# Kernel optimization log

Hardware: AMD Instinct MI355X
Metric: run time of the kernel (lower is better)

The kernel has to match this reference:

```python
import jax, jax.numpy as jnp
from jax import lax
import numpy as np

B, DM, NL, NC = 4, 256, 4, 1000
DI, NS, DTR, K = 512, 16, 32, 4  # d_inner, d_state, dt_rank, d_conv
EPS = 1e-5


def _bn(x, g, b):
    # eval-mode BatchNorm2d with running stats (mean=0, var=1)
    return x * (g / jnp.sqrt(1.0 + EPS))[None, :, None, None] + b[None, :, None, None]


def _conv2d(x, w, b, stride, pad):
    y = lax.conv_general_dilated(x, w, (stride, stride), pad,
                                 dimension_numbers=('NCHW', 'OIHW', 'NCHW'))
    return y + b[None, :, None, None]


def _ln(x, g, b):
    m = x.mean(-1, keepdims=True)
    v = ((x - m) ** 2).mean(-1, keepdims=True)
    return (x - m) / jnp.sqrt(v + EPS) * g + b


def _selective_scan(u, delta, A, Bm, Cm, D):
    # u, delta: [b,d,l]; A: [d,n]; Bm, Cm: [b,n,l]; D: [d]
    dA = jnp.exp(jnp.einsum('bdl,dn->lbdn', delta, A))        # [l,b,d,n]
    dBu = jnp.einsum('bdl,bnl,bdl->lbdn', delta, Bm, u)       # [l,b,d,n]
    h0 = jnp.zeros(dA.shape[1:], u.dtype)

    def step(h, inp):
        a, bu = inp
        h = a * h + bu
        return h, h

    _, hs = lax.scan(step, h0, (dA, dBu))                     # [l,b,d,n]
    y = jnp.einsum('lbdn,bnl->bdl', hs, Cm)
    return y + u * D[None, :, None]


def _mamba_block(x, ipw, ipb, cw, cb, xpw, dpw, dpb, alog, dssm, opw, opb):
    # x: [b,l,d_model]
    xr = x @ ipw.T + ipb                                      # [b,l,2*DI]
    xi, res = jnp.split(xr, 2, axis=-1)
    xc = jnp.swapaxes(xi, 1, 2)                               # [b,DI,l]
    # depthwise conv1d, kernel 4, torch padding='same' -> pad (1,2)
    xc = lax.conv_general_dilated(xc, cw, (1,), [(1, 2)],
                                  dimension_numbers=('NCW', 'OIW', 'NCW'),
                                  feature_group_count=DI) + cb[None, :, None]
    xl = jnp.swapaxes(xc, 1, 2)                               # [b,l,DI]
    xdbl = xl @ xpw.T                                         # [b,l,DTR+2*NS]
    d_dt, Bs, Cs = jnp.split(xdbl, [DTR, DTR + NS], axis=-1)
    delta = jax.nn.softplus(d_dt @ dpw.T + dpb)               # [b,l,DI]
    A = -jnp.exp(alog)                                        # [DI,NS]
    y = _selective_scan(jnp.swapaxes(xl, 1, 2), jnp.swapaxes(delta, 1, 2), A,
                        jnp.swapaxes(Bs, 1, 2), jnp.swapaxes(Cs, 1, 2), dssm)
    y = jnp.swapaxes(y, 1, 2)                                 # [b,l,DI]
    y = y * jax.nn.silu(res)
    return y @ opw.T + opb


def setup_inputs() -> dict:
    key = jax.random.key(0)
    ks = iter(jax.random.split(key, 32))

    def rn(shape, scale=0.02):
        return jax.random.normal(next(ks), shape, jnp.float32) * scale

    inp = {
        'x': jax.random.normal(next(ks), (B, 3, 64, 64), jnp.float32),
        # conv stem
        'c1w': rn((DM // 2, 3, 3, 3)), 'c1b': jnp.zeros((DM // 2,)),
        'g1': jnp.ones((DM // 2,)), 'b1': jnp.zeros((DM // 2,)),
        'c2w': rn((DM, DM // 2, 3, 3)), 'c2b': jnp.zeros((DM,)),
        'g2': jnp.ones((DM,)), 'b2': jnp.zeros((DM,)),
        'pw': rn((DM, DM, 2, 2)), 'pb': jnp.zeros((DM,)),
        'g3': jnp.ones((DM,)), 'b3': jnp.zeros((DM,)),
        # stacked mamba block params [NL, ...]
        'ipw': rn((NL, 2 * DI, DM)), 'ipb': jnp.zeros((NL, 2 * DI)),
        'cw': rn((NL, DI, 1, K), 0.1), 'cb': jnp.zeros((NL, DI)),
        'xpw': rn((NL, DTR + 2 * NS, DI)),
        'dpw': rn((NL, DI, DTR)), 'dpb': rn((NL, DI), 0.1),
        'alog': jnp.broadcast_to(jnp.log(jnp.arange(1, NS + 1, dtype=jnp.float32)), (NL, DI, NS)),
        'dssm': jnp.ones((NL, DI)),
        'opw': rn((NL, DM, DI)), 'opb': jnp.zeros((NL, DM)),
        'lnw': jnp.ones((NL, DM)), 'lnb': jnp.zeros((NL, DM)),
        # head
        'nw': jnp.ones((DM,)), 'nb': jnp.zeros((DM,)),
        'fcw': rn((NC, DM)), 'fcb': jnp.zeros((NC,)),
    }
    return inp


def reference(x, c1w, c1b, g1, b1, c2w, c2b, g2, b2, pw, pb, g3, b3,
              ipw, ipb, cw, cb, xpw, dpw, dpb, alog, dssm, opw, opb,
              lnw, lnb, nw, nb, fcw, fcb):
    h = _conv2d(x, c1w, c1b, 1, [(1, 1), (1, 1)])
    h = jax.nn.gelu(_bn(h, g1, b1), approximate=False)
    h = _conv2d(h, c2w, c2b, 1, [(1, 1), (1, 1)])
    h = jax.nn.gelu(_bn(h, g2, b2), approximate=False)
    h = _conv2d(h, pw, pb, 2, [(0, 0), (0, 0)])
    h = jax.nn.gelu(_bn(h, g3, b3), approximate=False)
    b, c, H, W = h.shape
    s = h.reshape(b, c, H * W).transpose(0, 2, 1)             # [b, L, d_model]
    for i in range(NL):
        y = _mamba_block(s, ipw[i], ipb[i], cw[i], cb[i], xpw[i], dpw[i],
                         dpb[i], alog[i], dssm[i], opw[i], opb[i])
        s = _ln(y, lnw[i], lnb[i]) + s
    s = s.mean(axis=1)
    s = _ln(s, nw, nb)
    logits = s @ fcw.T + fcb
    return logits, jax.nn.softmax(logits, axis=-1)
```

## Files before the change

### kernel.cpp

```cpp
#include <hip/hip_runtime.h>
#include <math.h>


#define BN_RSQ 0.99999500003749969f

typedef unsigned int uint;
typedef unsigned short ushort;
typedef __bf16 bf16x8 __attribute__((ext_vector_type(8)));
typedef float floatx4 __attribute__((ext_vector_type(4)));

__device__ __forceinline__ float gelu_f(float v) {
    return 0.5f * v * (1.0f + erff(v * 0.70710678118654752f));
}
__device__ __forceinline__ float softplus_f(float v) {
    return (v > 20.f) ? v : log1pf(expf(v));
}
__device__ __forceinline__ ushort f2bf(float f) {
    uint x = __float_as_uint(f);
    x += 0x7fffu + ((x >> 16) & 1u);
    return (ushort)(x >> 16);
}
__device__ __forceinline__ float bf2f(ushort u) {
    return __uint_as_float((uint)u << 16);
}

#define DPP_ROW_SHR_ADD(x, N)                                               \
    x += __int_as_float(__builtin_amdgcn_update_dpp(                        \
        0, __float_as_int(x), 0x110 + (N), 0xf, 0xf, true))

__global__ void wprep(const float* __restrict__ ipw, const float* __restrict__ opw,
                      const float* __restrict__ c2w, const float* __restrict__ pw,
                      const float* __restrict__ xpw,
                      ushort* __restrict__ ipwb, ushort* __restrict__ opwb,
                      ushort* __restrict__ w2b, ushort* __restrict__ pwTb,
                      ushort* __restrict__ xpwb)
{
    int idx = blockIdx.x * 256 + threadIdx.x;
    if (idx < 1048576) {
        ipwb[idx] = f2bf(ipw[idx]);
    } else if (idx < 1572864) {
        int i = idx - 1048576;
        opwb[i] = f2bf(opw[i]);
    } else if (idx < 1867776) {
        int i = idx - 1572864;
        int oc = i / 1152, k = i % 1152;
        int s = k >> 7, ic = k & 127;
        w2b[i] = f2bf(c2w[(size_t)(oc * 128 + ic) * 9 + s]);
    } else if (idx < 2129920) {
        int i = idx - 1867776;
        int oc = i >> 10, k = i & 1023;
        int s = k >> 8, ic = k & 255;
        int ky = s >> 1, kx = s & 1;
        pwTb[i] = f2bf(pw[((size_t)(oc * 256 + ic) * 2 + ky) * 2 + kx]);
    } else if (idx < 2260992) {
        int i = idx - 2129920;
        xpwb[i] = f2bf(xpw[i]);
    }
}

__global__ __launch_bounds__(256) void conv1_nhwc(
    const float* __restrict__ x, const float* __restrict__ w,
    const float* __restrict__ cb, const float* __restrict__ g,
    const float* __restrict__ bb, ushort* __restrict__ out)
{
    __shared__ float tin[3][3][64];
    __shared__ float ws[3456];
    int t = threadIdx.x;
    int b = blockIdx.x >> 6, y = blockIdx.x & 63;
    for (int i = t; i < 3456; i += 256) ws[i] = w[i];
    for (int i = t; i < 576; i += 256) {
        int ic = i / 192, r = (i >> 6) % 3, xx = i & 63;
        int gy = y + r - 1;
        tin[ic][r][xx] = ((unsigned)gy < 64u) ? x[((b * 3 + ic) * 64 + gy) * 64 + xx] : 0.f;
    }
    __syncthreads();
    int tx = t & 15, ty = t >> 4;
    int oc0 = tx * 8, px0 = ty * 4;
    float acc[4][8];
    #pragma unroll
    for (int p = 0; p < 4; ++p)
        #pragma unroll
        for (int o = 0; o < 8; ++o) acc[p][o] = 0.f;
    for (int ic = 0; ic < 3; ++ic)
        #pragma unroll
        for (int ky = 0; ky < 3; ++ky)
            #pragma unroll
            for (int kx = 0; kx < 3; ++kx) {
                float av[4];
                #pragma unroll
                for (int p = 0; p < 4; ++p) {
                    int xx = px0 + p + kx - 1;
                    av[p] = ((unsigned)xx < 64u) ? tin[ic][ky][xx] : 0.f;
                }
                #pragma unroll
                for (int o = 0; o < 8; ++o) {
                    float wv = ws[(oc0 + o) * 27 + ic * 9 + ky * 3 + kx];
                    #pragma unroll
                    for (int p = 0; p < 4; ++p) acc[p][o] = fmaf(av[p], wv, acc[p][o]);
                }
            }
    #pragma unroll
    for (int p = 0; p < 4; ++p) {
        uint pk[4];
        #pragma unroll
        for (int o2 = 0; o2 < 4; ++o2) {
            int oc = oc0 + o2 * 2;
            float v0 = gelu_f((acc[p][o2 * 2] + cb[oc]) * (g[oc] * BN_RSQ) + bb[oc]);
            float v1 = gelu_f((acc[p][o2 * 2 + 1] + cb[oc + 1]) * (g[oc + 1] * BN_RSQ) + bb[oc + 1]);
            pk[o2] = (uint)f2bf(v0) | ((uint)f2bf(v1) << 16);
        }
        uint4 vv = make_uint4(pk[0], pk[1], pk[2], pk[3]);
        *(uint4*)(out + ((size_t)((b * 64 + y) * 64 + px0 + p)) * 128 + oc0) = vv;
    }
}

template<int BM, int BN, int EPI>
__global__ __launch_bounds__(256, 2) void mfma_gemm_bt(
    const ushort* __restrict__ A, int lda,
    const ushort* __restrict__ W, int ldw,
    const float* __restrict__ bias,
    const float* __restrict__ bnG, const float* __restrict__ bnB,
    float* __restrict__ Cf, ushort* __restrict__ Cb, ushort* __restrict__ Cb2,
    int ldc, int K)
{
    constexpr int PAD = 40;
    constexpr int AP = BM / 64;
    constexpr int BP = BN / 64;
    constexpr int FM = BM / 32;
    constexpr int FN = BN / 32;
    __shared__ __align__(16) ushort As[BM * PAD];
    __shared__ __align__(16) ushort Bs[BN * PAD];
    int t = threadIdx.x;
    int m0 = blockIdx.x * BM, n0 = blockIdx.y * BN;
    int lane = t & 63, wid = t >> 6;
    int wm = (wid & 1) * (BM / 2), wn = (wid >> 1) * (BN / 2);
    int fr = lane & 15, fk = (lane >> 4) * 8;
    int r0 = t >> 2, c0 = (t & 3) * 8;
    floatx4 acc[FM][FN];
    #pragma unroll
    for (int i = 0; i < FM; ++i)
        #pragma unroll
        for (int j = 0; j < FN; ++j) acc[i][j] = {0.f, 0.f, 0.f, 0.f};
    uint4 ra[AP], rb[BP];
    #pragma unroll
    for (int p = 0; p < AP; ++p)
        ra[p] = *(const uint4*)(A + (size_t)(m0 + r0 + p * 64) * lda + c0);
    #pragma unroll
    for (int p = 0; p < BP; ++p)
        rb[p] = *(const uint4*)(W + (size_t)(n0 + r0 + p * 64) * ldw + c0);
    for (int k0 = 0; k0 < K; k0 += 32) {
        __syncthreads();
        #pragma unroll
        for (int p = 0; p < AP; ++p) *(uint4*)&As[(r0 + p * 64) * PAD + c0] = ra[p];
        #pragma unroll
        for (int p = 0; p < BP; ++p) *(uint4*)&Bs[(r0 + p * 64) * PAD + c0] = rb[p];
        __syncthreads();
        if (k0 + 32 < K) {
            #pragma unroll
            for (int p = 0; p < AP; ++p)
                ra[p] = *(const uint4*)(A + (size_t)(m0 + r0 + p * 64) * lda + k0 + 32 + c0);
            #pragma unroll
            for (int p = 0; p < BP; ++p)
                rb[p] = *(const uint4*)(W + (size_t)(n0 + r0 + p * 64) * ldw + k0 + 32 + c0);
        }
        bf16x8 af[FM], bw[FN];
        #pragma unroll
        for (int i = 0; i < FM; ++i)
            af[i] = *(const bf16x8*)&As[(wm + i * 16 + fr) * PAD + fk];
        #pragma unroll
        for (int j = 0; j < FN; ++j)
            bw[j] = *(const bf16x8*)&Bs[(wn + j * 16 + fr) * PAD + fk];
        #pragma unroll
        for (int i = 0; i < FM; ++i)
            #pragma unroll
            for (int j = 0; j < FN; ++j)
                acc[i][j] = __builtin_amdgcn_mfma_f32_16x16x32_bf16(af[i], bw[j], acc[i][j], 0, 0, 0);
    }
    int rbase = (lane >> 4) * 4, cc = lane & 15;
    #pragma unroll
    for (int j = 0; j < FN; ++j) {
        int n = n0 + wn + j * 16 + cc;
        float bv = bias ? bias[n] : 0.f;
        float scl = 0.f, shf = 0.f;
        if (EPI == 2) { scl = bnG[n] * BN_RSQ; shf = bnB[n]; }
        #pragma unroll
        for (int i = 0; i < FM; ++i) {
            #pragma unroll
            for (int r = 0; r < 4; ++r) {
                int m = m0 + wm + i * 16 + rbase + r;
                float v = acc[i][j][r] + bv;
                if (EPI == 2) v = gelu_f(v * scl + shf);
                if (EPI == 0) {
                    Cf[(size_t)m * ldc + n] = v;
                } else if (EPI == 2) {
                    Cf[(size_t)m * ldc + n] = v;
                    Cb[(size_t)m * ldc + n] = f2bf(v);
                } else {
                    if (n < 512) Cb[(size_t)m * 512 + n] = f2bf(v);
                    else Cb2[(size_t)m * 512 + (n - 512)] = f2bf(v / (1.f + __expf(-v)));
                }
            }
        }
    }
}

#define C2_LOAD(step)                                                            \
    {                                                                            \
        int s_ = (step) >> 1, ich_ = ((step) & 1) * 64;                          \
        int ky_ = s_ / 3, kx_ = s_ % 3;                                          \
        int sy_ = y0 + (ra_row >> 6) + ky_ - 1;                                  \
        int sx_ = (ra_row & 63) + kx_ - 1;                                       \
        bool v_ = ((unsigned)sy_ < 64u) && ((unsigned)sx_ < 64u);                \
        const ushort* ap_ = hb + ((size_t)(sy_ * 64 + sx_)) * 128 + ich_ + ra_c; \
        uint4 zz_ = make_uint4(0u, 0u, 0u, 0u);                                  \
        ra0 = v_ ? *(const uint4*)(ap_ + 0)  : zz_;                              \
        ra1 = v_ ? *(const uint4*)(ap_ + 8)  : zz_;                              \
        ra2 = v_ ? *(const uint4*)(ap_ + 16) : zz_;                              \
        ra3 = v_ ? *(const uint4*)(ap_ + 24) : zz_;                              \
        const ushort* wp_ = w2b + (size_t)(n0 + rb_row) * 1152 + s_ * 128 + ich_ + rb_c; \
        rb0 = *(const uint4*)(wp_ + 0);                                          \
        rb1 = *(const uint4*)(wp_ + 8);                                          \
    }

__global__ __launch_bounds__(256, 2) void conv2_mfma(
    const ushort* __restrict__ h1b, const ushort* __restrict__ w2b,
    const float* __restrict__ cb, const float* __restrict__ g,
    const float* __restrict__ bb, ushort* __restrict__ h2b)
{
    constexpr int PAD = 72;
    __shared__ __align__(16) ushort As[128 * PAD];
    __shared__ __align__(16) ushort Bs[64 * PAD];
    int t = threadIdx.x;
    int m0 = blockIdx.x * 128, n0 = blockIdx.y * 64;
    int b = m0 >> 12;
    int y0 = (m0 & 4095) >> 6;
    int lane = t & 63, wid = t >> 6;
    int wm = (wid & 1) * 64, wn = (wid >> 1) * 32;
    int fr = lane & 15, fk = (lane >> 4) * 8;
    int ra_row = t >> 1, ra_c = (t & 1) * 32;
    int rb_row = t >> 2, rb_c = (t & 3) * 16;
    floatx4 acc[4][2];
    #pragma unroll
    for (int i = 0; i < 4; ++i)
        #pragma unroll
        for (int j = 0; j < 2; ++j) acc[i][j] = {0.f, 0.f, 0.f, 0.f};
    const ushort* hb = h1b + (size_t)b * 4096 * 128;

    uint4 ra0, ra1, ra2, ra3, rb0, rb1;
    C2_LOAD(0);
    for (int step = 0; step < 18; ++step) {
        __syncthreads();
        *(uint4*)&As[ra_row * PAD + ra_c + 0]  = ra0;
        *(uint4*)&As[ra_row * PAD + ra_c + 8]  = ra1;
        *(uint4*)&As[ra_row * PAD + ra_c + 16] = ra2;
        *(uint4*)&As[ra_row * PAD + ra_c + 24] = ra3;
        *(uint4*)&Bs[rb_row * PAD + rb_c + 0]  = rb0;
        *(uint4*)&Bs[rb_row * PAD + rb_c + 8]  = rb1;
        __syncthreads();
        if (step + 1 < 18) C2_LOAD(step + 1);
        #pragma unroll
        for (int ks = 0; ks < 64; ks += 32) {
            bf16x8 af[4], bw[2];
            #pragma unroll
            for (int i = 0; i < 4; ++i)
                af[i] = *(const bf16x8*)&As[(wm + i * 16 + fr) * PAD + ks + fk];
            #pragma unroll
            for (int j = 0; j < 2; ++j)
                bw[j] = *(const bf16x8*)&Bs[(wn + j * 16 + fr) * PAD + ks + fk];
            #pragma unroll
            for (int i = 0; i < 4; ++i)
                #pragma unroll
                for (int j = 0; j < 2; ++j)
                    acc[i][j] = __builtin_amdgcn_mfma_f32_16x16x32_bf16(af[i], bw[j], acc[i][j], 0, 0, 0);
        }
    }
    int rbase = (lane >> 4) * 4, cc = lane & 15;
    #pragma unroll
    for (int j = 0; j < 2; ++j) {
        int n = n0 + wn + j * 16 + cc;
        float scl = g[n] * BN_RSQ, shf = bb[n], bv2 = cb[n];
        #pragma unroll
        for (int i = 0; i < 4; ++i) {
            #pragma unroll
            for (int r = 0; r < 4; ++r) {
                int m = m0 + wm + i * 16 + rbase + r;
                float v = gelu_f((acc[i][j][r] + bv2) * scl + shf);
                h2b[(size_t)m * 256 + n] = f2bf(v);
            }
        }
    }
}

__global__ void im2col_bf16(const ushort* __restrict__ h2b, ushort* __restrict__ Apb)
{
    int idx = blockIdx.x * 256 + threadIdx.x;
    int k8 = idx & 127;
    int m = idx >> 7;
    int b = m >> 10, oy = (m >> 5) & 31, ox = m & 31;
    int s = k8 >> 5, ic8 = k8 & 31;
    int ky = s >> 1, kx = s & 1;
    uint4 v = *(const uint4*)(h2b + ((size_t)(b * 4096 + (2 * oy + ky) * 64 + 2 * ox + kx)) * 256 + ic8 * 8);
    *(uint4*)(Apb + (size_t)m * 1024 + k8 * 8) = v;
}

template<int BM, int BN, int BK, int TM, int TN>
__global__ __launch_bounds__(256) void gemm_kernel(
    const float* __restrict__ A, int lda,
    const float* __restrict__ W, int ldw,
    const float* __restrict__ bias,
    float* __restrict__ C, int ldc,
    int M, int N, int K, int act)
{
    static_assert(BM * BK / 4 == 256 && BN * BK / 4 == 256, "staging shape");
    __shared__ float As[BK][BM + 4];
    __shared__ float Bs[BK][BN + 4];
    int t = threadIdx.x;
    int m0 = blockIdx.x * BM, n0 = blockIdx.y * BN;
    float acc[TM][TN];
    #pragma unroll
    for (int i = 0; i < TM; i++)
        #pragma unroll
        for (int j = 0; j < TN; j++) acc[i][j] = 0.f;
    const int LPR = BK / 4;
    int lr = t / LPR, lc4 = (t % LPR) * 4;
    int ty = t >> 4, tx = t & 15;
    int ma = m0 + lr, nb = n0 + lr;
    float4 va = make_float4(0.f, 0.f, 0.f, 0.f);
    float4 vb = make_float4(0.f, 0.f, 0.f, 0.f);
    if (ma < M) va = *(const float4*)(A + (size_t)ma * lda + lc4);
    if (nb < N) vb = *(const float4*)(W + (size_t)nb * ldw + lc4);
    for (int k0 = 0; k0 < K; k0 += BK) {
        __syncthreads();
        As[lc4 + 0][lr] = va.x; As[lc4 + 1][lr] = va.y;
        As[lc4 + 2][lr] = va.z; As[lc4 + 3][lr] = va.w;
        Bs[lc4 + 0][lr] = vb.x; Bs[lc4 + 1][lr] = vb.y;
        Bs[lc4 + 2][lr] = vb.z; Bs[lc4 + 3][lr] = vb.w;
        __syncthreads();
        if (k0 + BK < K) {
            if (ma < M) va = *(const float4*)(A + (size_t)ma * lda + k0 + BK + lc4);
            if (nb < N) vb = *(const float4*)(W + (size_t)nb * ldw + k0 + BK + lc4);
        }
        #pragma unroll
        for (int kk = 0; kk < BK; ++kk) {
            float a[TM], bfr[TN];
            #pragma unroll
            for (int i = 0; i < TM; i += 4)
                *(float4*)&a[i] = *(const float4*)&As[kk][ty * TM + i];
            #pragma unroll
            for (int j = 0; j < TN; j += 4)
                *(float4*)&bfr[j] = *(const float4*)&Bs[kk][tx * TN + j];
            #pragma unroll
            for (int i = 0; i < TM; i++)
                #pragma unroll
                for (int j = 0; j < TN; j++) acc[i][j] = fmaf(a[i], bfr[j], acc[i][j]);
        }
    }
    #pragma unroll
    for (int i = 0; i < TM; i++) {
        int m = m0 + ty * TM + i;
        if (m >= M) continue;
        #pragma unroll
        for (int j = 0; j < TN; j++) {
            int n = n0 + tx * TN + j;
            if (n >= N) continue;
            float v = acc[i][j];
            if (bias) v += bias[n];
            if (act == 2) v = softplus_f(v);
            C[(size_t)m * ldc + n] = v;
        }
    }
}

__global__ __launch_bounds__(256) void dwconv(
    const ushort* __restrict__ xib, const float* __restrict__ cw,
    const float* __restrict__ cb, ushort* __restrict__ xlb)
{
    int idx = blockIdx.x * 256 + threadIdx.x;
    int d4 = (idx & 127) * 4;
    int bl = idx >> 7;
    int b = bl >> 10, l = bl & 1023;
    float4 w0 = *(const float4*)(cw + d4 * 4);
    float4 w1 = *(const float4*)(cw + d4 * 4 + 4);
    float4 w2 = *(const float4*)(cw + d4 * 4 + 8);
    float4 w3 = *(const float4*)(cw + d4 * 4 + 12);
    float4 acc = *(const float4*)(cb + d4);
    const ushort* rowb = xib + ((size_t)b << 19) + d4;
    #pragma unroll
    for (int k = 0; k < 4; ++k) {
        int ll = l + k - 1;
        if ((unsigned)ll < 1024u) {
            uint2 p = *(const uint2*)(rowb + (size_t)ll * 512);
            acc.x = fmaf(bf2f((ushort)(p.x & 0xffffu)), ((const float*)&w0)[k], acc.x);
            acc.y = fmaf(bf2f((ushort)(p.x >> 16)),     ((const float*)&w1)[k], acc.y);
            acc.z = fmaf(bf2f((ushort)(p.y & 0xffffu)), ((const float*)&w2)[k], acc.z);
            acc.w = fmaf(bf2f((ushort)(p.y >> 16)),     ((const float*)&w3)[k], acc.w);
        }
    }
    uint2 pk;
    pk.x = (uint)f2bf(acc.x) | ((uint)f2bf(acc.y) << 16);
    pk.y = (uint)f2bf(acc.z) | ((uint)f2bf(acc.w) << 16);
    *(uint2*)(xlb + (size_t)bl * 512 + d4) = pk;
}

__global__ __launch_bounds__(512, 8) void scan_part1(
    const float* __restrict__ xdbl, const ushort* __restrict__ xlb,
    const float* __restrict__ dpw, const float* __restrict__ dpb,
    const float* __restrict__ alog,
    float* __restrict__ Psum, float* __restrict__ hFsum)
{
    __shared__ __align__(16) float Td[32][68];
    __shared__ __align__(16) float Tu[32][68];
    __shared__ __align__(16) float TB[16][68];
    __shared__ __align__(16) float xd[64][32];
    __shared__ float dpw_s[32][33];
    __shared__ float dpb_s[32];
    int t = threadIdx.x;
    int bid = blockIdx.x;
    int ch = bid % 15;
    int gq = bid / 15;
    int dgG = gq & 15, b = gq >> 4;
    int d0 = dgG * 32;
    int bl0 = b * 1024 + ch * 64;
    {
        int l = t >> 3, k4 = (t & 7) * 4;
        float4 v = *(const float4*)(xdbl + (size_t)(bl0 + l) * 64 + k4);
        *(float4*)&xd[l][k4] = v;
    }
    if (t < 256) {
        int l = t >> 2, d8 = (t & 3) * 8;
        uint4 p = *(const uint4*)(xlb + (size_t)(bl0 + l) * 512 + d0 + d8);
        Tu[d8 + 0][l] = bf2f((ushort)(p.x & 0xffffu));
        Tu[d8 + 1][l] = bf2f((ushort)(p.x >> 16));
        Tu[d8 + 2][l] = bf2f((ushort)(p.y & 0xffffu));
        Tu[d8 + 3][l] = bf2f((ushort)(p.y >> 16));
        Tu[d8 + 4][l] = bf2f((ushort)(p.z & 0xffffu));
        Tu[d8 + 5][l] = bf2f((ushort)(p.z >> 16));
        Tu[d8 + 6][l] = bf2f((ushort)(p.w & 0xffffu));
        Tu[d8 + 7][l] = bf2f((ushort)(p.w >> 16));
    } else {
        int tt = t - 256;
        int l = tt >> 2, n4 = (tt & 3) * 4;
        float4 bv = *(const float4*)(xdbl + (size_t)(bl0 + l) * 64 + 32 + n4);
        TB[n4 + 0][l] = bv.x; TB[n4 + 1][l] = bv.y;
        TB[n4 + 2][l] = bv.z; TB[n4 + 3][l] = bv.w;
    }
    #pragma unroll
    for (int r = 0; r < 2; ++r) {
        int idx = r * 512 + t;
        int dd = idx >> 5, kk = idx & 31;
        dpw_s[dd][kk] = dpw[(size_t)(d0 + dd) * 32 + kk];
    }
    if (t < 32) dpb_s[t] = dpb[d0 + t];
    __syncthreads();
    {
        int dd = t & 31, lb = (t >> 5) * 4;
        #pragma unroll
        for (int j = 0; j < 4; ++j) {
            int l = lb + j;
            float s = dpb_s[dd];
            #pragma unroll
            for (int k = 0; k < 32; ++k) s = fmaf(xd[l][k], dpw_s[dd][k], s);
            Td[dd][l] = softplus_f(s);
        }
    }
    __syncthreads();
    int w = t >> 6, lane = t & 63;
    int dl = lane >> 4, n = lane & 15;
    int col = w * 4 + dl;
    int d = d0 + col;
    float Ac = -__expf(alog[d * 16 + n]);
    float h = 0.f, P = 1.f;
    for (int l4 = 0; l4 < 16; ++l4) {
        float4 de = *(const float4*)&Td[col][l4 * 4];
        float4 uu = *(const float4*)&Tu[col][l4 * 4];
        float4 Bv = *(const float4*)&TB[n][l4 * 4];
        float a1 = __expf(de.x * Ac), a2 = __expf(de.y * Ac);
        float a3 = __expf(de.z * Ac), a4 = __expf(de.w * Ac);
        float b1 = de.x * Bv.x * uu.x, b2 = de.y * Bv.y * uu.y;
        float b3 = de.z * Bv.z * uu.z, b4 = de.w * Bv.w * uu.w;
        float a21 = a2 * a1,     b21 = fmaf(a2, b1, b2);
        float a321 = a3 * a21,   b321 = fmaf(a3, b21, b3);
        float a4321 = a4 * a321, b4321 = fmaf(a4, b321, b4);
        h = fmaf(a4321, h, b4321);
        P *= a4321;
    }
    size_t si = ((size_t)(b * 128 + dgG * 8 + w) * 16 + ch) * 64 + lane;
    Psum[si] = P;
    hFsum[si] = h;
}

__global__ __launch_bounds__(512, 8) void scan_part2(
    const float* __restrict__ xdbl, const ushort* __restrict__ xlb,
    const float* __restrict__ dpw, const float* __restrict__ dpb,
    const float* __restrict__ alog, const float* __restrict__ dssm,
    const ushort* __restrict__ resb, ushort* __restrict__ ybb,
    const float* __restrict__ Psum, const float* __restrict__ hFsum)
{
    __shared__ __align__(16) float Td[32][68];
    __shared__ __align__(16) float Tu[32][68];
    __shared__ __align__(16) unsigned char uni[12928];
    __shared__ float dpw_s[32][33];
    __shared__ float dpb_s[32];
    float* xd = (float*)uni;
    float (*TB)[68] = (float(*)[68])uni;
    float (*TC)[68] = (float(*)[68])(uni + 4352);
    uint (*yb2)[33] = (uint(*)[33])(uni + 8704);
    int t = threadIdx.x;
    int bid = blockIdx.x;
    int ch = bid & 15, dgG = (bid >> 4) & 15, b = bid >> 8;
    int d0 = dgG * 32;
    int bl0 = b * 1024 + ch * 64;
    {
        int l = t >> 3, k4 = (t & 7) * 4;
        float4 v = *(const float4*)(xdbl + (size_t)(bl0 + l) * 64 + k4);
        *(float4*)&xd[l * 32 + k4] = v;
    }
    if (t < 256) {
        int l = t >> 2, d8 = (t & 3) * 8;
        uint4 p = *(const uint4*)(xlb + (size_t)(bl0 + l) * 512 + d0 + d8);
        Tu[d8 + 0][l] = bf2f((ushort)(p.x & 0xffffu));
        Tu[d8 + 1][l] = bf2f((ushort)(p.x >> 16));
        Tu[d8 + 2][l] = bf2f((ushort)(p.y & 0xffffu));
        Tu[d8 + 3][l] = bf2f((ushort)(p.y >> 16));
        Tu[d8 + 4][l] = bf2f((ushort)(p.z & 0xffffu));
        Tu[d8 + 5][l] = bf2f((ushort)(p.z >> 16));
        Tu[d8 + 6][l] = bf2f((ushort)(p.w & 0xffffu));
        Tu[d8 + 7][l] = bf2f((ushort)(p.w >> 16));
    }
    #pragma unroll
    for (int r = 0; r < 2; ++r) {
        int idx = r * 512 + t;
        int dd = idx >> 5, kk = idx & 31;
        dpw_s[dd][kk] = dpw[(size_t)(d0 + dd) * 32 + kk];
    }
    if (t < 32) dpb_s[t] = dpb[d0 + t];
    __syncthreads();
    {
        int dd = t & 31, lb = (t >> 5) * 4;
        #pragma unroll
        for (int j = 0; j < 4; ++j) {
            int l = lb + j;
            float s = dpb_s[dd];
            #pragma unroll
            for (int k = 0; k < 32; ++k) s = fmaf(xd[l * 32 + k], dpw_s[dd][k], s);
            Td[dd][l] = softplus_f(s);
        }
    }
    __syncthreads();
    if (t < 256) {
        int l = t >> 2, n4 = (t & 3) * 4;
        float4 bv = *(const float4*)(xdbl + (size_t)(bl0 + l) * 64 + 32 + n4);
        float4 cv = *(const float4*)(xdbl + (size_t)(bl0 + l) * 64 + 48 + n4);
        TB[n4 + 0][l] = bv.x; TB[n4 + 1][l] = bv.y;
        TB[n4 + 2][l] = bv.z; TB[n4 + 3][l] = bv.w;
        TC[n4 + 0][l] = cv.x; TC[n4 + 1][l] = cv.y;
        TC[n4 + 2][l] = cv.z; TC[n4 + 3][l] = cv.w;
    }
    int w = t >> 6, lane = t & 63;
    int dl = lane >> 4, n = lane & 15;
    int col = w * 4 + dl;
    int d = d0 + col;
    float Ac = -__expf(alog[d * 16 + n]);
    float Dd = dssm[d];
    float h = 0.f;
    {
        size_t sbase = (size_t)(b * 128 + dgG * 8 + w) * 1024 + lane;
        for (int cc = 0; cc < ch; ++cc) {
            float Pv = Psum[sbase + (size_t)cc * 64];
            float hv = hFsum[sbase + (size_t)cc * 64];
            h = Pv * h + hv;
        }
    }
    __syncthreads();
    for (int l4 = 0; l4 < 16; ++l4) {
        float4 de = *(const float4*)&Td[col][l4 * 4];
        float4 uu = *(const float4*)&Tu[col][l4 * 4];
        float4 Bv = *(const float4*)&TB[n][l4 * 4];
        float4 Cv = *(const float4*)&TC[n][l4 * 4];
        float a1 = __expf(de.x * Ac), a2 = __expf(de.y * Ac);
        float a3 = __expf(de.z * Ac), a4 = __expf(de.w * Ac);
        float b1 = de.x * Bv.x * uu.x, b2 = de.y * Bv.y * uu.y;
        float b3 = de.z * Bv.z * uu.z, b4 = de.w * Bv.w * uu.w;
        float a21 = a2 * a1,     b21 = fmaf(a2, b1, b2);
        float a321 = a3 * a21,   b321 = fmaf(a3, b21, b3);
        float a4321 = a4 * a321, b4321 = fmaf(a4, b321, b4);
        float h1 = fmaf(a1, h, b1);
        float h2 = fmaf(a21, h, b21);
        float h3 = fmaf(a321, h, b321);
        float h4 = fmaf(a4321, h, b4321);
        h = h4;
        float p0 = h1 * Cv.x, p1 = h2 * Cv.y, p2 = h3 * Cv.z, p3 = h4 * Cv.w;
        DPP_ROW_SHR_ADD(p0, 1); DPP_ROW_SHR_ADD(p0, 2);
        DPP_ROW_SHR_ADD(p0, 4); DPP_ROW_SHR_ADD(p0, 8);
        DPP_ROW_SHR_ADD(p1, 1); DPP_ROW_SHR_ADD(p1, 2);
        DPP_ROW_SHR_ADD(p1, 4); DPP_ROW_SHR_ADD(p1, 8);
        DPP_ROW_SHR_ADD(p2, 1); DPP_ROW_SHR_ADD(p2, 2);
        DPP_ROW_SHR_ADD(p2, 4); DPP_ROW_SHR_ADD(p2, 8);
        DPP_ROW_SHR_ADD(p3, 1); DPP_ROW_SHR_ADD(p3, 2);
        DPP_ROW_SHR_ADD(p3, 4); DPP_ROW_SHR_ADD(p3, 8);
        if (n == 15) {
            int l2 = l4 * 2;
            float y0 = fmaf(uu.x, Dd, p0), y1 = fmaf(uu.y, Dd, p1);
            float y2 = fmaf(uu.z, Dd, p2), y3 = fmaf(uu.w, Dd, p3);
            yb2[l2 + 0][col] = (uint)f2bf(y0) | ((uint)f2bf(y1) << 16);
            yb2[l2 + 1][col] = (uint)f2bf(y2) | ((uint)f2bf(y3) << 16);
        }
    }
    __syncthreads();
    size_t base = ((size_t)(b * 1024 + ch * 64)) * 512 + d0;
    #pragma unroll
    for (int j = 0; j < 2; ++j) {
        int idx = j * 512 + t;
        int l2 = idx >> 5, col2 = idx & 31;
        uint yv = yb2[l2][col2];
        int l0 = l2 * 2;
        float r0 = bf2f(resb[base + (size_t)l0 * 512 + col2]);
        float r1 = bf2f(resb[base + (size_t)(l0 + 1) * 512 + col2]);
        float y0 = bf2f((ushort)(yv & 0xffffu)) * r0;
        float y1 = bf2f((ushort)(yv >> 16)) * r1;
        ybb[base + (size_t)l0 * 512 + col2] = f2bf(y0);
        ybb[base + (size_t)(l0 + 1) * 512 + col2] = f2bf(y1);
    }
}

__global__ __launch_bounds__(256) void ln_res_kernel(
    const float* __restrict__ o, const float* __restrict__ g,
    const float* __restrict__ bb, float* __restrict__ s, ushort* __restrict__ sb)
{
    int row = blockIdx.x * 4 + (threadIdx.x >> 6);
    int lane = threadIdx.x & 63;
    const float4* orow = (const float4*)(o + (size_t)row * 256);
    float4 v = orow[lane];
    float sum = v.x + v.y + v.z + v.w;
    float sq = v.x * v.x + v.y * v.y + v.z * v.z + v.w * v.w;
    #pragma unroll
    for (int off = 1; off < 64; off <<= 1) {
        sum += __shfl_xor(sum, off);
        sq += __shfl_xor(sq, off);
    }
    float m = sum * (1.f / 256.f);
    float var = sq * (1.f / 256.f) - m * m;
    float rstd = rsqrtf(var + 1e-5f);
    float4 gg = ((const float4*)g)[lane];
    float4 bv = ((const float4*)bb)[lane];
    float4* srow = (float4*)(s + (size_t)row * 256);
    float4 sv = srow[lane];
    sv.x += (v.x - m) * rstd * gg.x + bv.x;
    sv.y += (v.y - m) * rstd * gg.y + bv.y;
    sv.z += (v.z - m) * rstd * gg.z + bv.z;
    sv.w += (v.w - m) * rstd * gg.w + bv.w;
    srow[lane] = sv;
    uint2 pk;
    pk.x = (uint)f2bf(sv.x) | ((uint)f2bf(sv.y) << 16);
    pk.y = (uint)f2bf(sv.z) | ((uint)f2bf(sv.w) << 16);
    *(uint2*)(sb + (size_t)row * 256 + lane * 4) = pk;
}

__global__ __launch_bounds__(256) void pool_ln_kernel(
    const float* __restrict__ s, const float* __restrict__ nw,
    const float* __restrict__ nb, float* __restrict__ sln)
{
    int b = blockIdx.x, c = threadIdx.x;
    const float* p = s + (size_t)b * 262144 + c;
    float acc = 0.f;
    for (int l = 0; l < 1024; ++l) acc += p[(size_t)l * 256];
    float pooled = acc * (1.f / 1024.f);
    __shared__ float rs[4], rq[4];
    float sum = pooled, sq = pooled * pooled;
    #pragma unroll
    for (int off = 1; off < 64; off <<= 1) {
        sum += __shfl_xor(sum, off);
        sq += __shfl_xor(sq, off);
    }
    int w = threadIdx.x >> 6;
    if ((threadIdx.x & 63) == 0) { rs[w] = sum; rq[w] = sq; }
    __syncthreads();
    sum = rs[0] + rs[1] + rs[2] + rs[3];
    sq = rq[0] + rq[1] + rq[2] + rq[3];
    float m = sum * (1.f / 256.f);
    float var = sq * (1.f / 256.f) - m * m;
    float rstd = rsqrtf(var + 1e-5f);
    sln[b * 256 + c] = (pooled - m) * rstd * nw[c] + nb[c];
}

__global__ __launch_bounds__(256) void softmax_kernel(float* __restrict__ out)
{
    int b = threadIdx.x >> 6, lane = threadIdx.x & 63;
    const float* lg = out + b * 1000;
    float v[16];
    float mx = -1e30f;
    #pragma unroll
    for (int j = 0; j < 16; ++j) {
        int i = lane + j * 64;
        v[j] = (i < 1000) ? lg[i] : -1e30f;
        mx = fmaxf(mx, v[j]);
    }
    #pragma unroll
    for (int off = 1; off < 64; off <<= 1) mx = fmaxf(mx, __shfl_xor(mx, off));
    float sum = 0.f;
    #pragma unroll
    for (int j = 0; j < 16; ++j) {
        int i = lane + j * 64;
        if (i < 1000) { v[j] = __expf(v[j] - mx); sum += v[j]; }
    }
    #pragma unroll
    for (int off = 1; off < 64; off <<= 1) sum += __shfl_xor(sum, off);
    float inv = 1.f / sum;
    float* so = out + 4000 + b * 1000;
    #pragma unroll
    for (int j = 0; j < 16; ++j) {
        int i = lane + j * 64;
        if (i < 1000) so[i] = v[j] * inv;
    }
}

extern "C" void kernel_launch(void* const* d_in, const int* in_sizes, int n_in,
                              void* d_out, int out_size, void* d_ws, size_t ws_size,
                              hipStream_t stream)
{
    const float* x    = (const float*)d_in[0];
    const float* c1w  = (const float*)d_in[1];
    const float* c1b  = (const float*)d_in[2];
    const float* g1   = (const float*)d_in[3];
    const float* b1   = (const float*)d_in[4];
    const float* c2w  = (const float*)d_in[5];
    const float* c2b  = (const float*)d_in[6];
    const float* g2   = (const float*)d_in[7];
    const float* b2   = (const float*)d_in[8];
    const float* pw   = (const float*)d_in[9];
    const float* pb   = (const float*)d_in[10];
    const float* g3   = (const float*)d_in[11];
    const float* b3   = (const float*)d_in[12];
    const float* ipw  = (const float*)d_in[13];
    const float* ipb  = (const float*)d_in[14];
    const float* cw   = (const float*)d_in[15];
    const float* cb   = (const float*)d_in[16];
    const float* xpw  = (const float*)d_in[17];
    const float* dpw  = (const float*)d_in[18];
    const float* dpb  = (const float*)d_in[19];
    const float* alog = (const float*)d_in[20];
    const float* dssm = (const float*)d_in[21];
    const float* opw  = (const float*)d_in[22];
    const float* opb  = (const float*)d_in[23];
    const float* lnw  = (const float*)d_in[24];
    const float* lnb  = (const float*)d_in[25];
    const float* nw   = (const float*)d_in[26];
    const float* nb   = (const float*)d_in[27];
    const float* fcw  = (const float*)d_in[28];
    const float* fcb  = (const float*)d_in[29];
    float* out = (float*)d_out;
    float* wsf = (float*)d_ws;

    float*  s_   = wsf;
    ushort* sb   = (ushort*)(wsf + 1048576);
    ushort* xib  = (ushort*)(wsf + 1572864);
    ushort* h2b  = (ushort*)(wsf + 1572864);
    float*  obuf = wsf + 1572864;
    ushort* resb = (ushort*)(wsf + 3670016);
    ushort* xlb  = (ushort*)(wsf + 4718592);
    ushort* ybb  = (ushort*)(wsf + 4718592);
    ushort* h1b  = (ushort*)(wsf + 4718592);
    ushort* Apb  = (ushort*)(wsf + 6815744);
    float*  xdbl = wsf + 8912896;
    ushort* ipwb = (ushort*)(wsf + 9175040);
    ushort* opwb = (ushort*)(wsf + 9699328);
    ushort* w2b  = (ushort*)(wsf + 9961472);
    ushort* pwTb = (ushort*)(wsf + 10108928);
    float*  sln  = wsf + 10240000;
    float*  Psum = wsf + 10241024;
    float*  hFsum= wsf + 10765312;
    ushort* xpwb = (ushort*)(wsf + 11289600);

    hipLaunchKernelGGL(wprep, dim3(8832), dim3(256), 0, stream,
                       ipw, opw, c2w, pw, xpw, ipwb, opwb, w2b, pwTb, xpwb);

    hipLaunchKernelGGL(conv1_nhwc, dim3(256), dim3(256), 0, stream, x, c1w, c1b, g1, b1, h1b);
    hipLaunchKernelGGL(conv2_mfma, dim3(128, 4), dim3(256), 0, stream, h1b, w2b, c2b, g2, b2, h2b);
    hipLaunchKernelGGL(im2col_bf16, dim3(2048), dim3(256), 0, stream, h2b, Apb);
    hipLaunchKernelGGL((mfma_gemm_bt<64, 64, 2>), dim3(64, 4), dim3(256), 0, stream,
                       Apb, 1024, pwTb, 1024, pb, g3, b3, s_, sb, nullptr, 256, 1024);

    for (int i = 0; i < 4; ++i) {
        const ushort* ipwb_i = ipwb + (size_t)i * 1024 * 256;
        const float*  ipb_i  = ipb + i * 1024;
        const float*  cw_i   = cw + i * 512 * 4;
        const float*  cb_i   = cb + i * 512;
        const ushort* xpwb_i = xpwb + (size_t)i * 64 * 512;
        const float*  dpw_i  = dpw + (size_t)i * 512 * 32;
        const float*  dpb_i  = dpb + i * 512;
        const float*  alog_i = alog + (size_t)i * 512 * 16;
        const float*  dssm_i = dssm + i * 512;
        const ushort* opwb_i = opwb + (size_t)i * 256 * 512;
        const float*  opb_i  = opb + i * 256;
        const float*  lnw_i  = lnw + i * 256;
        const float*  lnb_i  = lnb + i * 256;

        hipLaunchKernelGGL((mfma_gemm_bt<64, 128, 3>), dim3(64, 8), dim3(256), 0, stream,
                           sb, 256, ipwb_i, 256, ipb_i, nullptr, nullptr,
                           nullptr, xib, resb, 0, 256);
        hipLaunchKernelGGL(dwconv, dim3(2048), dim3(256), 0, stream, xib, cw_i, cb_i, xlb);
        hipLaunchKernelGGL((mfma_gemm_bt<64, 64, 0>), dim3(64, 1), dim3(256), 0, stream,
                           xlb, 512, xpwb_i, 512, nullptr, nullptr, nullptr,
                           xdbl, nullptr, nullptr, 64, 512);
        hipLaunchKernelGGL(scan_part1, dim3(960), dim3(512), 0, stream,
                           xdbl, xlb, dpw_i, dpb_i, alog_i, Psum, hFsum);
        hipLaunchKernelGGL(scan_part2, dim3(1024), dim3(512), 0, stream,
                           xdbl, xlb, dpw_i, dpb_i, alog_i, dssm_i, resb, ybb, Psum, hFsum);
        hipLaunchKernelGGL((mfma_gemm_bt<64, 64, 0>), dim3(64, 4), dim3(256), 0, stream,
                           ybb, 512, opwb_i, 512, opb_i, nullptr, nullptr,
                           obuf, nullptr, nullptr, 256, 512);
        hipLaunchKernelGGL(ln_res_kernel, dim3(1024), dim3(256), 0, stream,
                           obuf, lnw_i, lnb_i, s_, sb);
    }

    hipLaunchKernelGGL(pool_ln_kernel, dim3(4), dim3(256), 0, stream, s_, nw, nb, sln);
    hipLaunchKernelGGL((gemm_kernel<64, 64, 16, 4, 4>), dim3(1, 16), dim3(256), 0, stream,
                       sln, 256, fcw, 256, fcb, out, 1000, 4, 1000, 256, 0);
    hipLaunchKernelGGL(softmax_kernel, dim3(1), dim3(256), 0, stream, out);
}
```

Measured before the change: 594.6 us.

## Compute delta once in scan pass 1 and reuse it from global in pass 2

Measured after the change: 1.197 ms. +101.3%, slower.

```diff
diff --git a/kernel.cpp b/kernel.cpp
--- a/kernel.cpp
+++ b/kernel.cpp
@@ -406,25 +406,24 @@
     const float* __restrict__ xdbl, const ushort* __restrict__ xlb,
     const float* __restrict__ dpw, const float* __restrict__ dpb,
     const float* __restrict__ alog,
-    float* __restrict__ Psum, float* __restrict__ hFsum)
+    float* __restrict__ Psum, float* __restrict__ hFsum, float* __restrict__ Tdg)
 {
     __shared__ __align__(16) float Td[32][68];
+    __shared__ __align__(16) float xdt[32][68];
     __shared__ __align__(16) float Tu[32][68];
     __shared__ __align__(16) float TB[16][68];
-    __shared__ __align__(16) float xd[64][32];
-    __shared__ float dpw_s[32][33];
+    __shared__ float dpwt[32][33];
     __shared__ float dpb_s[32];
     int t = threadIdx.x;
     int bid = blockIdx.x;
-    int ch = bid % 15;
-    int gq = bid / 15;
-    int dgG = gq & 15, b = gq >> 4;
+    int ch = bid & 15, dgG = (bid >> 4) & 15, b = bid >> 8;
     int d0 = dgG * 32;
     int bl0 = b * 1024 + ch * 64;
     {
         int l = t >> 3, k4 = (t & 7) * 4;
         float4 v = *(const float4*)(xdbl + (size_t)(bl0 + l) * 64 + k4);
-        *(float4*)&xd[l][k4] = v;
+        xdt[k4 + 0][l] = v.x; xdt[k4 + 1][l] = v.y;
+        xdt[k4 + 2][l] = v.z; xdt[k4 + 3][l] = v.w;
     }
     if (t < 256) {
         int l = t >> 2, d8 = (t & 3) * 8;
@@ -447,23 +446,31 @@
     #pragma unroll
     for (int r = 0; r < 2; ++r) {
         int idx = r * 512 + t;
-        int dd = idx >> 5, kk = idx & 31;
-        dpw_s[dd][kk] = dpw[(size_t)(d0 + dd) * 32 + kk];
+        int dd2 = idx >> 5, kk = idx & 31;
+        dpwt[kk][dd2] = dpw[(size_t)(d0 + dd2) * 32 + kk];
     }
     if (t < 32) dpb_s[t] = dpb[d0 + t];
     __syncthreads();
     {
         int dd = t & 31, lb = (t >> 5) * 4;
-        #pragma unroll
-        for (int j = 0; j < 4; ++j) {
-            int l = lb + j;
-            float s = dpb_s[dd];
-            #pragma unroll
-            for (int k = 0; k < 32; ++k) s = fmaf(xd[l][k], dpw_s[dd][k], s);
-            Td[dd][l] = softplus_f(s);
-        }
+        float s0 = dpb_s[dd], s1 = s0, s2 = s0, s3 = s0;
+        #pragma unroll
+        for (int k = 0; k < 32; ++k) {
+            float w = dpwt[k][dd];
+            float4 xv = *(const float4*)&xdt[k][lb];
+            s0 = fmaf(xv.x, w, s0); s1 = fmaf(xv.y, w, s1);
+            s2 = fmaf(xv.z, w, s2); s3 = fmaf(xv.w, w, s3);
+        }
+        float4 tv = make_float4(softplus_f(s0), softplus_f(s1),
+                                softplus_f(s2), softplus_f(s3));
+        *(float4*)&Td[dd][lb] = tv;
     }
     __syncthreads();
+    {
+        int row = t >> 4, c4 = (t & 15) * 4;
+        float4 tv = *(const float4*)&Td[row][c4];
+        *(float4*)(Tdg + ((size_t)((b * 16 + dgG) * 32 + row)) * 1024 + ch * 64 + c4) = tv;
+    }
     int w = t >> 6, lane = t & 63;
     int dl = lane >> 4, n = lane & 15;
     int col = w * 4 + dl;
@@ -490,30 +497,27 @@
 }
 
 __global__ __launch_bounds__(512, 8) void scan_part2(
-    const float* __restrict__ xdbl, const ushort* __restrict__ xlb,
-    const float* __restrict__ dpw, const float* __restrict__ dpb,
+    const float* __restrict__ Tdg, const ushort* __restrict__ xlb,
+    const float* __restrict__ xdbl,
     const float* __restrict__ alog, const float* __restrict__ dssm,
     const ushort* __restrict__ resb, ushort* __restrict__ ybb,
     const float* __restrict__ Psum, const float* __restrict__ hFsum)
 {
     __shared__ __align__(16) float Td[32][68];
     __shared__ __align__(16) float Tu[32][68];
-    __shared__ __align__(16) unsigned char uni[12928];
-    __shared__ float dpw_s[32][33];
-    __shared__ float dpb_s[32];
-    float* xd = (float*)uni;
-    float (*TB)[68] = (float(*)[68])uni;
-    float (*TC)[68] = (float(*)[68])(uni + 4352);
-    uint (*yb2)[33] = (uint(*)[33])(uni + 8704);
+    __shared__ __align__(16) float TB[16][68];
+    __shared__ __align__(16) float TC[16][68];
+    __shared__ __align__(8) uint yb2[32][33];
     int t = threadIdx.x;
     int bid = blockIdx.x;
     int ch = bid & 15, dgG = (bid >> 4) & 15, b = bid >> 8;
     int d0 = dgG * 32;
     int bl0 = b * 1024 + ch * 64;
     {
-        int l = t >> 3, k4 = (t & 7) * 4;
-        float4 v = *(const float4*)(xdbl + (size_t)(bl0 + l) * 64 + k4);
-        *(float4*)&xd[l * 32 + k4] = v;
+        int row = t >> 4, c4 = (t & 15) * 4;
+        float4 tv = *(const float4*)(Tdg +
+            ((size_t)((b * 16 + dgG) * 32 + row)) * 1024 + ch * 64 + c4);
+        *(float4*)&Td[row][c4] = tv;
     }
     if (t < 256) {
         int l = t >> 2, d8 = (t & 3) * 8;
@@ -526,29 +530,9 @@
         Tu[d8 + 5][l] = bf2f((ushort)(p.z >> 16));
         Tu[d8 + 6][l] = bf2f((ushort)(p.w & 0xffffu));
         Tu[d8 + 7][l] = bf2f((ushort)(p.w >> 16));
-    }
-    #pragma unroll
-    for (int r = 0; r < 2; ++r) {
-        int idx = r * 512 + t;
-        int dd = idx >> 5, kk = idx & 31;
-        dpw_s[dd][kk] = dpw[(size_t)(d0 + dd) * 32 + kk];
-    }
-    if (t < 32) dpb_s[t] = dpb[d0 + t];
-    __syncthreads();
-    {
-        int dd = t & 31, lb = (t >> 5) * 4;
-        #pragma unroll
-        for (int j = 0; j < 4; ++j) {
-            int l = lb + j;
-            float s = dpb_s[dd];
-            #pragma unroll
-            for (int k = 0; k < 32; ++k) s = fmaf(xd[l * 32 + k], dpw_s[dd][k], s);
-            Td[dd][l] = softplus_f(s);
-        }
-    }
-    __syncthreads();
-    if (t < 256) {
-        int l = t >> 2, n4 = (t & 3) * 4;
+    } else {
+        int tt = t - 256;
+        int l = tt >> 2, n4 = (tt & 3) * 4;
         float4 bv = *(const float4*)(xdbl + (size_t)(bl0 + l) * 64 + 32 + n4);
         float4 cv = *(const float4*)(xdbl + (size_t)(bl0 + l) * 64 + 48 + n4);
         TB[n4 + 0][l] = bv.x; TB[n4 + 1][l] = bv.y;
@@ -565,10 +549,14 @@
     float h = 0.f;
     {
         size_t sbase = (size_t)(b * 128 + dgG * 8 + w) * 1024 + lane;
-        for (int cc = 0; cc < ch; ++cc) {
+        #pragma unroll
+        for (int cc = 0; cc < 15; ++cc) {
             float Pv = Psum[sbase + (size_t)cc * 64];
             float hv = hFsum[sbase + (size_t)cc * 64];
-            h = Pv * h + hv;
+            bool use = cc < ch;
+            Pv = use ? Pv : 1.f;
+            hv = use ? hv : 0.f;
+            h = fmaf(Pv, h, hv);
         }
     }
     __syncthreads();
@@ -770,6 +758,7 @@
     float*  Psum = wsf + 10241024;
     float*  hFsum= wsf + 10765312;
     ushort* xpwb = (ushort*)(wsf + 11289600);
+    float*  Tdg  = wsf + 11355136;
 
     hipLaunchKernelGGL(wprep, dim3(8832), dim3(256), 0, stream,
                        ipw, opw, c2w, pw, xpw, ipwb, opwb, w2b, pwTb, xpwb);
@@ -802,10 +791,10 @@
         hipLaunchKernelGGL((mfma_gemm_bt<64, 64, 0>), dim3(64, 1), dim3(256), 0, stream,
                            xlb, 512, xpwb_i, 512, nullptr, nullptr, nullptr,
                            xdbl, nullptr, nullptr, 64, 512);
-        hipLaunchKernelGGL(scan_part1, dim3(960), dim3(512), 0, stream,
-                           xdbl, xlb, dpw_i, dpb_i, alog_i, Psum, hFsum);
+        hipLaunchKernelGGL(scan_part1, dim3(1024), dim3(512), 0, stream,
+                           xdbl, xlb, dpw_i, dpb_i, alog_i, Psum, hFsum, Tdg);
         hipLaunchKernelGGL(scan_part2, dim3(1024), dim3(512), 0, stream,
-                           xdbl, xlb, dpw_i, dpb_i, alog_i, dssm_i, resb, ybb, Psum, hFsum);
+                           Tdg, xlb, xdbl, alog_i, dssm_i, resb, ybb, Psum, hFsum);
         hipLaunchKernelGGL((mfma_gemm_bt<64, 64, 0>), dim3(64, 4), dim3(256), 0, stream,
                            ybb, 512, opwb_i, 512, opb_i, nullptr, nullptr,
                            obuf, nullptr, nullptr, 256, 512);
```
